# Optimization experiments

Hardware: AMD Instinct MI355X
Metric: run time of the kernel (lower is better)

The kernel has to match this reference:

```python
import jax, jax.numpy as jnp
import numpy as np

W_BIT = 4
A_BIT = 8
Q_GROUP_SIZE = 128  # weight quant group size along in_features


def _fake_quant_ste(t, n_bits, zero_point, q_group_size):
    """Per-group fake quant with straight-through estimator."""
    shape = t.shape
    if q_group_size > 0:
        q = t.reshape(-1, q_group_size)
    else:
        q = t.reshape(-1, shape[-1])
    if zero_point:
        max_val = jnp.max(q, axis=1, keepdims=True)
        min_val = jnp.min(q, axis=1, keepdims=True)
        max_int = 2 ** n_bits - 1
        min_int = 0
        scales = jnp.clip(max_val - min_val, 1e-5, None) / max_int
        zeros = jnp.clip(-jnp.round(min_val / scales), min_int, max_int)
    else:
        max_val = jnp.clip(jnp.max(jnp.abs(q), axis=1, keepdims=True), 1e-5, None)
        max_int = 2 ** (n_bits - 1) - 1
        min_int = -(2 ** (n_bits - 1))
        scales = max_val / max_int
        zeros = 0.0
    dq = (jnp.clip(jnp.round(q / scales) + zeros, min_int, max_int) - zeros) * scales
    dq = dq.reshape(shape)
    # STE: identity gradient through the quantizer
    return t + jax.lax.stop_gradient(dq - t)


def setup_inputs() -> dict:
    key = jax.random.key(0)
    k1, k2, k3, k4 = jax.random.split(key, 4)
    B, S, D_IN, D_OUT = 4, 2048, 4096, 4096
    x = jax.random.normal(k1, (B, S, D_IN), dtype=jnp.float32)
    weight = jax.random.normal(k2, (D_OUT, D_IN), dtype=jnp.float32) * 0.02
    bias = jax.random.normal(k3, (D_OUT,), dtype=jnp.float32) * 0.01
    log_scale = jax.random.normal(k4, (D_IN,), dtype=jnp.float32) * 0.1
    return {"x": x, "weight": weight, "bias": bias, "log_scale": log_scale}


def reference(x, weight, bias, log_scale):
    scale = jnp.clip(jnp.exp(log_scale), 1e-4, 1e4)  # [D_IN]
    x = x / scale                                    # broadcast over last dim
    weight = weight * scale[None, :]                 # [D_OUT, D_IN]
    # per-token (last-dim) symmetric activation quant
    xq = _fake_quant_ste(x, A_BIT, zero_point=False, q_group_size=-1)
    # per-group asymmetric weight quant
    wq = _fake_quant_ste(weight, W_BIT, zero_point=True, q_group_size=Q_GROUP_SIZE)
    # F.linear: x @ W^T + b
    return jnp.einsum("bsd,od->bso", xq, wq) + bias
```

## Files before the change

### kernel.cpp

```cpp
#include <hip/hip_runtime.h>
#include <hip/hip_bf16.h>
#include <cstdint>
#include <cstddef>

#define D_IN  4096
#define D_OUT 4096
#define M_TOK 8192
#define QG    128

typedef __bf16 bf16x8 __attribute__((ext_vector_type(8)));
typedef float  floatx4 __attribute__((ext_vector_type(4)));

__global__ __launch_bounds__(256) void scale_kernel(const float* __restrict__ ls,
                                                    float* __restrict__ scale) {
    int i = blockIdx.x * 256 + threadIdx.x;
    if (i < D_IN) {
        float s = expf(ls[i]);
        s = fminf(fmaxf(s, 1e-4f), 1e4f);
        scale[i] = s;
    }
}

__global__ __launch_bounds__(256) void act_quant(const float* __restrict__ x,
                                                 const float* __restrict__ scale,
                                                 __hip_bfloat16* __restrict__ xq) {
    const int row = blockIdx.x;
    const int tid = threadIdx.x;
    const float* xr = x + (size_t)row * D_IN;

    float v[16];
    float amax = 0.f;
#pragma unroll
    for (int i = 0; i < 16; ++i) {
        int d = tid + i * 256;
        float q = xr[d] / scale[d];
        v[i] = q;
        amax = fmaxf(amax, fabsf(q));
    }
#pragma unroll
    for (int off = 32; off > 0; off >>= 1)
        amax = fmaxf(amax, __shfl_xor(amax, off, 64));
    __shared__ float smax[4];
    if ((tid & 63) == 0) smax[tid >> 6] = amax;
    __syncthreads();
    float m = fmaxf(fmaxf(smax[0], smax[1]), fmaxf(smax[2], smax[3]));
    m = fmaxf(m, 1e-5f);
    const float s = m / 127.0f;

    __hip_bfloat16* xo = xq + (size_t)row * D_IN;
#pragma unroll
    for (int i = 0; i < 16; ++i) {
        int d = tid + i * 256;
        float dq = fminf(fmaxf(rintf(v[i] / s), -128.f), 127.f) * s;
        xo[d] = __float2bfloat16(dq);
    }
}

__global__ __launch_bounds__(256) void w_quant(const float* __restrict__ wgt,
                                               const float* __restrict__ scale,
                                               __hip_bfloat16* __restrict__ wq) {
    const int gid  = blockIdx.x * 4 + (threadIdx.x >> 6);
    const int lane = threadIdx.x & 63;
    const size_t e0 = (size_t)gid * QG + lane * 2;
    const int d0 = (int)(e0 & (D_IN - 1));

    float2 wv = *(const float2*)(wgt + e0);
    float w0 = wv.x * scale[d0];
    float w1 = wv.y * scale[d0 + 1];

    float mx = fmaxf(w0, w1), mn = fminf(w0, w1);
#pragma unroll
    for (int off = 32; off > 0; off >>= 1) {
        mx = fmaxf(mx, __shfl_xor(mx, off, 64));
        mn = fminf(mn, __shfl_xor(mn, off, 64));
    }
    const float s = fmaxf(mx - mn, 1e-5f) / 15.0f;
    const float z = fminf(fmaxf(-rintf(mn / s), 0.f), 15.f);

    float dq0 = (fminf(fmaxf(rintf(w0 / s) + z, 0.f), 15.f) - z) * s;
    float dq1 = (fminf(fmaxf(rintf(w1 / s) + z, 0.f), 15.f) - z) * s;

    __hip_bfloat162 h;
    h.x = __float2bfloat16(dq0);
    h.y = __float2bfloat16(dq1);
    *(__hip_bfloat162*)(wq + e0) = h;
}

__global__ __launch_bounds__(256) void gemm_bt(const __hip_bfloat16* __restrict__ A,
                                               const __hip_bfloat16* __restrict__ B,
                                               const float* __restrict__ bias,
                                               float* __restrict__ C) {
    constexpr int K = D_IN;
    __shared__ unsigned short Alds[128 * 32];
    __shared__ unsigned short Blds[128 * 32];

    const int tid  = threadIdx.x;
    const int lane = tid & 63;
    const int w    = tid >> 6;
    const int bn   = blockIdx.x;
    const int bm   = blockIdx.y;
    const int wm   = (w >> 1) * 64;
    const int wn   = (w & 1) * 64;
    const int q    = lane >> 4;
    const int l16  = lane & 15;

    floatx4 acc[4][4] = {};

    for (int k0 = 0; k0 < K; k0 += 32) {
        __syncthreads();
#pragma unroll
        for (int t = 0; t < 2; ++t) {
            int f = t * 256 + tid;
            int r = f >> 2, c = f & 3;
            const __hip_bfloat16* ga = A + (size_t)(bm * 128 + r) * K + k0 + c * 8;
            __builtin_amdgcn_global_load_lds(
                (const __attribute__((address_space(1))) void*)ga,
                (__attribute__((address_space(3))) void*)(Alds + f * 8), 16, 0, 0);
            const __hip_bfloat16* gb = B + (size_t)(bn * 128 + r) * K + k0 + c * 8;
            __builtin_amdgcn_global_load_lds(
                (const __attribute__((address_space(1))) void*)gb,
                (__attribute__((address_space(3))) void*)(Blds + f * 8), 16, 0, 0);
        }
        __syncthreads();

        bf16x8 af[4], bfr[4];
#pragma unroll
        for (int i = 0; i < 4; ++i) {
            af[i]  = *(const bf16x8*)(Alds + (wm + i * 16 + l16) * 32 + q * 8);
            bfr[i] = *(const bf16x8*)(Blds + (wn + i * 16 + l16) * 32 + q * 8);
        }
#pragma unroll
        for (int mi = 0; mi < 4; ++mi)
#pragma unroll
            for (int ni = 0; ni < 4; ++ni)
                acc[mi][ni] = __builtin_amdgcn_mfma_f32_16x16x32_bf16(
                    af[mi], bfr[ni], acc[mi][ni], 0, 0, 0);
    }

    float bv[4];
#pragma unroll
    for (int ni = 0; ni < 4; ++ni)
        bv[ni] = bias[bn * 128 + wn + ni * 16 + l16];

#pragma unroll
    for (int mi = 0; mi < 4; ++mi) {
        int gm = bm * 128 + wm + mi * 16 + q * 4;
#pragma unroll
        for (int ni = 0; ni < 4; ++ni) {
            int gn = bn * 128 + wn + ni * 16 + l16;
            float* cp = C + (size_t)gm * D_OUT + gn;
#pragma unroll
            for (int r = 0; r < 4; ++r)
                cp[(size_t)r * D_OUT] = acc[mi][ni][r] + bv[ni];
        }
    }
}

extern "C" void kernel_launch(void* const* d_in, const int* in_sizes, int n_in,
                              void* d_out, int out_size, void* d_ws, size_t ws_size,
                              hipStream_t stream) {
    const float* x   = (const float*)d_in[0];
    const float* wgt = (const float*)d_in[1];
    const float* bia = (const float*)d_in[2];
    const float* ls  = (const float*)d_in[3];
    float* out = (float*)d_out;

    char* ws = (char*)d_ws;
    float*          scale = (float*)ws;
    __hip_bfloat16* xq    = (__hip_bfloat16*)(ws + (64 << 10));
    __hip_bfloat16* wq    = (__hip_bfloat16*)(ws + (64 << 10) + ((size_t)64 << 20));

    scale_kernel<<<(D_IN + 255) / 256, 256, 0, stream>>>(ls, scale);
    act_quant<<<M_TOK, 256, 0, stream>>>(x, scale, xq);
    w_quant<<<(D_OUT * D_IN / QG) / 4, 256, 0, stream>>>(wgt, scale, wq);

    dim3 grid(D_OUT / 128, M_TOK / 128);
    gemm_bt<<<grid, 256, 0, stream>>>(xq, wq, bia, out);
}
```

Before: 576.6 us.

## Vectorize quant kernels, use reciprocal multiplies, and swizzle GEMM LDS layout

```diff
diff --git a/kernel.cpp b/kernel.cpp
--- a/kernel.cpp
+++ b/kernel.cpp
@@ -12,30 +12,35 @@
 typedef float  floatx4 __attribute__((ext_vector_type(4)));
 
 __global__ __launch_bounds__(256) void scale_kernel(const float* __restrict__ ls,
-                                                    float* __restrict__ scale) {
+                                                    float* __restrict__ scale,
+                                                    float* __restrict__ rinv) {
     int i = blockIdx.x * 256 + threadIdx.x;
     if (i < D_IN) {
         float s = expf(ls[i]);
         s = fminf(fmaxf(s, 1e-4f), 1e4f);
         scale[i] = s;
+        rinv[i]  = 1.0f / s;
     }
 }
 
 __global__ __launch_bounds__(256) void act_quant(const float* __restrict__ x,
-                                                 const float* __restrict__ scale,
+                                                 const float* __restrict__ rinv,
                                                  __hip_bfloat16* __restrict__ xq) {
     const int row = blockIdx.x;
     const int tid = threadIdx.x;
-    const float* xr = x + (size_t)row * D_IN;
+    const float4* xr = (const float4*)(x + (size_t)row * D_IN);
+    const float4* rv = (const float4*)rinv;
 
     float v[16];
     float amax = 0.f;
 #pragma unroll
-    for (int i = 0; i < 16; ++i) {
-        int d = tid + i * 256;
-        float q = xr[d] / scale[d];
-        v[i] = q;
-        amax = fmaxf(amax, fabsf(q));
+    for (int j = 0; j < 4; ++j) {
+        int idx = j * 256 + tid;
+        float4 xv = xr[idx];
+        float4 ri = rv[idx];
+        float a = xv.x * ri.x, b = xv.y * ri.y, c = xv.z * ri.z, d = xv.w * ri.w;
+        v[j * 4 + 0] = a; v[j * 4 + 1] = b; v[j * 4 + 2] = c; v[j * 4 + 3] = d;
+        amax = fmaxf(amax, fmaxf(fmaxf(fabsf(a), fabsf(b)), fmaxf(fabsf(c), fabsf(d))));
     }
 #pragma unroll
     for (int off = 32; off > 0; off >>= 1)
@@ -45,45 +50,53 @@
     __syncthreads();
     float m = fmaxf(fmaxf(smax[0], smax[1]), fmaxf(smax[2], smax[3]));
     m = fmaxf(m, 1e-5f);
-    const float s = m / 127.0f;
+    const float s  = m / 127.0f;
+    const float qs = 1.0f / s;
 
-    __hip_bfloat16* xo = xq + (size_t)row * D_IN;
+    ushort4* xo = (ushort4*)(xq + (size_t)row * D_IN);
 #pragma unroll
-    for (int i = 0; i < 16; ++i) {
-        int d = tid + i * 256;
-        float dq = fminf(fmaxf(rintf(v[i] / s), -128.f), 127.f) * s;
-        xo[d] = __float2bfloat16(dq);
+    for (int j = 0; j < 4; ++j) {
+        union { ushort4 u; __hip_bfloat16 h[4]; } p;
+#pragma unroll
+        for (int k = 0; k < 4; ++k) {
+            float dq = fminf(fmaxf(rintf(v[j * 4 + k] * qs), -128.f), 127.f) * s;
+            p.h[k] = __float2bfloat16(dq);
+        }
+        xo[j * 256 + tid] = p.u;
     }
 }
 
 __global__ __launch_bounds__(256) void w_quant(const float* __restrict__ wgt,
                                                const float* __restrict__ scale,
                                                __hip_bfloat16* __restrict__ wq) {
-    const int gid  = blockIdx.x * 4 + (threadIdx.x >> 6);
+    const int wid  = blockIdx.x * 4 + (threadIdx.x >> 6);
     const int lane = threadIdx.x & 63;
-    const size_t e0 = (size_t)gid * QG + lane * 2;
+    const size_t e0 = (size_t)wid * 256 + lane * 4;
     const int d0 = (int)(e0 & (D_IN - 1));
 
-    float2 wv = *(const float2*)(wgt + e0);
-    float w0 = wv.x * scale[d0];
-    float w1 = wv.y * scale[d0 + 1];
+    float4 wv = *(const float4*)(wgt + e0);
+    float4 sv = *(const float4*)(scale + d0);
+    float w0 = wv.x * sv.x, w1 = wv.y * sv.y, w2 = wv.z * sv.z, w3 = wv.w * sv.w;
 
-    float mx = fmaxf(w0, w1), mn = fminf(w0, w1);
+    float mx = fmaxf(fmaxf(w0, w1), fmaxf(w2, w3));
+    float mn = fminf(fminf(w0, w1), fminf(w2, w3));
 #pragma unroll
-    for (int off = 32; off > 0; off >>= 1) {
+    for (int off = 16; off > 0; off >>= 1) {
         mx = fmaxf(mx, __shfl_xor(mx, off, 64));
         mn = fminf(mn, __shfl_xor(mn, off, 64));
     }
-    const float s = fmaxf(mx - mn, 1e-5f) / 15.0f;
-    const float z = fminf(fmaxf(-rintf(mn / s), 0.f), 15.f);
+    const float s  = fmaxf(mx - mn, 1e-5f) / 15.0f;
+    const float rs = 1.0f / s;
+    const float z  = fminf(fmaxf(-rintf(mn * rs), 0.f), 15.f);
 
-    float dq0 = (fminf(fmaxf(rintf(w0 / s) + z, 0.f), 15.f) - z) * s;
-    float dq1 = (fminf(fmaxf(rintf(w1 / s) + z, 0.f), 15.f) - z) * s;
-
-    __hip_bfloat162 h;
-    h.x = __float2bfloat16(dq0);
-    h.y = __float2bfloat16(dq1);
-    *(__hip_bfloat162*)(wq + e0) = h;
+    union { ushort4 u; __hip_bfloat16 h[4]; } p;
+    float wl[4] = {w0, w1, w2, w3};
+#pragma unroll
+    for (int k = 0; k < 4; ++k) {
+        float dq = (fminf(fmaxf(rintf(wl[k] * rs) + z, 0.f), 15.f) - z) * s;
+        p.h[k] = __float2bfloat16(dq);
+    }
+    *(ushort4*)(wq + e0) = p.u;
 }
 
 __global__ __launch_bounds__(256) void gemm_bt(const __hip_bfloat16* __restrict__ A,
@@ -103,6 +116,8 @@
     const int wn   = (w & 1) * 64;
     const int q    = lane >> 4;
     const int l16  = lane & 15;
+    const int sw   = (l16 >> 1) & 3;
+    const int colOff = ((q ^ sw)) * 8;
 
     floatx4 acc[4][4] = {};
 
@@ -111,7 +126,8 @@
 #pragma unroll
         for (int t = 0; t < 2; ++t) {
             int f = t * 256 + tid;
-            int r = f >> 2, c = f & 3;
+            int r = f >> 2;
+            int c = (f & 3) ^ ((f >> 3) & 3);
             const __hip_bfloat16* ga = A + (size_t)(bm * 128 + r) * K + k0 + c * 8;
             __builtin_amdgcn_global_load_lds(
                 (const __attribute__((address_space(1))) void*)ga,
@@ -126,8 +142,8 @@
         bf16x8 af[4], bfr[4];
 #pragma unroll
         for (int i = 0; i < 4; ++i) {
-            af[i]  = *(const bf16x8*)(Alds + (wm + i * 16 + l16) * 32 + q * 8);
-            bfr[i] = *(const bf16x8*)(Blds + (wn + i * 16 + l16) * 32 + q * 8);
+            af[i]  = *(const bf16x8*)(Alds + (wm + i * 16 + l16) * 32 + colOff);
+            bfr[i] = *(const bf16x8*)(Blds + (wn + i * 16 + l16) * 32 + colOff);
         }
 #pragma unroll
         for (int mi = 0; mi < 4; ++mi)
@@ -167,12 +183,13 @@
 
     char* ws = (char*)d_ws;
     float*          scale = (float*)ws;
+    float*          rinv  = (float*)(ws + (16 << 10));
     __hip_bfloat16* xq    = (__hip_bfloat16*)(ws + (64 << 10));
     __hip_bfloat16* wq    = (__hip_bfloat16*)(ws + (64 << 10) + ((size_t)64 << 20));
 
-    scale_kernel<<<(D_IN + 255) / 256, 256, 0, stream>>>(ls, scale);
-    act_quant<<<M_TOK, 256, 0, stream>>>(x, scale, xq);
-    w_quant<<<(D_OUT * D_IN / QG) / 4, 256, 0, stream>>>(wgt, scale, wq);
+    scale_kernel<<<(D_IN + 255) / 256, 256, 0, stream>>>(ls, scale, rinv);
+    act_quant<<<M_TOK, 256, 0, stream>>>(x, rinv, xq);
+    w_quant<<<(D_OUT * D_IN / 256) / 4, 256, 0, stream>>>(wgt, scale, wq);
 
     dim3 grid(D_OUT / 128, M_TOK / 128);
     gemm_bt<<<grid, 256, 0, stream>>>(xq, wq, bia, out);
```

After: 569.8 us. Within noise of the previous version (-1.2%).
